# Kernel optimization log

Measured on AMD Instinct MI355X. Metric: run time of the kernel, lower is better.

The kernel has to match this reference:

```python
import jax, jax.numpy as jnp
import numpy as np

IN_DIM, HID, NCLS = 384, 16, 2
BN_EPS = 1e-5

def setup_inputs() -> dict:
    key = jax.random.key(0)
    ks = jax.random.split(key, 10)
    N, E, G = 50000, 200000, 64
    x = jax.random.normal(ks[0], (N, IN_DIM), dtype=jnp.float32)
    edge_index = jax.random.randint(ks[1], (2, E), 0, N, dtype=jnp.int64)
    batch = jnp.sort(jax.random.randint(ks[2], (N,), 0, G, dtype=jnp.int64))
    s1 = 1.0 / np.sqrt(2 * IN_DIM)
    s2 = 1.0 / np.sqrt(IN_DIM)
    s3 = 1.0 / np.sqrt(HID)
    lin_l_w = jax.random.uniform(ks[3], (HID, 2 * IN_DIM), minval=-s1, maxval=s1, dtype=jnp.float32)
    lin_l_b = jax.random.uniform(ks[4], (HID,), minval=-s1, maxval=s1, dtype=jnp.float32)
    lin_r_w = jax.random.uniform(ks[5], (HID, IN_DIM), minval=-s2, maxval=s2, dtype=jnp.float32)
    bn_gamma = jnp.ones((HID,), dtype=jnp.float32)
    bn_beta = jnp.zeros((HID,), dtype=jnp.float32)
    fc_w = jax.random.uniform(ks[6], (NCLS, HID), minval=-s3, maxval=s3, dtype=jnp.float32)
    fc_b = jax.random.uniform(ks[7], (NCLS,), minval=-s3, maxval=s3, dtype=jnp.float32)
    return {"x": x, "edge_index": edge_index, "batch": batch, "num_graphs": G,
            "lin_l_w": lin_l_w, "lin_l_b": lin_l_b, "lin_r_w": lin_r_w,
            "bn_gamma": bn_gamma, "bn_beta": bn_beta, "fc_w": fc_w, "fc_b": fc_b}

def reference(x, edge_index, batch, num_graphs, lin_l_w, lin_l_b, lin_r_w, bn_gamma, bn_beta, fc_w, fc_b):
    N = x.shape[0]
    # flow='target_to_source': aggregate x[edge_index[1]] (j) onto edge_index[0] (i)
    i, j = edge_index[0], edge_index[1]
    msg = x[j]                                                    # [E, IN_DIM]
    sum_agg = jax.ops.segment_sum(msg, i, num_segments=N)        # [N, IN_DIM]
    cnt = jax.ops.segment_sum(jnp.ones((msg.shape[0],), x.dtype), i, num_segments=N)
    mean_agg = sum_agg / jnp.clip(cnt, 1.0)[:, None]
    max_agg = jax.ops.segment_max(msg, i, num_segments=N)        # -inf where empty
    max_agg = jnp.where(jnp.isfinite(max_agg), max_agg, 0.0)     # PyG leaves 0 for isolated nodes
    agg = jnp.concatenate([mean_agg, max_agg], axis=-1)          # [N, 2*IN_DIM] (MultiAggregation cat)
    h = agg @ lin_l_w.T + lin_l_b + x @ lin_r_w.T                # SAGEConv: lin_l(aggr) + lin_r(root)
    # BatchNorm1d, training-mode batch statistics (biased variance)
    mu = jnp.mean(h, axis=0)
    var = jnp.mean(jnp.square(h - mu), axis=0)
    h = (h - mu) * jax.lax.rsqrt(var + BN_EPS) * bn_gamma + bn_beta
    h = jax.nn.relu(h)                                           # [N, HID]; hierarchical cat of 1 layer = h
    # global_mean_pool
    pooled_sum = jax.ops.segment_sum(h, batch, num_segments=num_graphs)
    gcnt = jax.ops.segment_sum(jnp.ones((N,), h.dtype), batch, num_segments=num_graphs)
    pooled = pooled_sum / jnp.clip(gcnt, 1.0)[:, None]           # [G, HID]
    return pooled @ fc_w.T + fc_b                                # [G, NCLS]
```

## Files before the change

kernel.cpp:

```cpp
#include <hip/hip_runtime.h>
#include <hip/hip_bf16.h>
#include <math.h>

#define IN_DIM 384
#define HID 16
#define NCLS 2
#define BN_EPS 1e-5f
#define MAXG 64
#define SLOTS 64

typedef __attribute__((ext_vector_type(8))) short bf16x8;
typedef __attribute__((ext_vector_type(4))) float f32x4;

__device__ __forceinline__ unsigned packbf(float a, float b) {
    __hip_bfloat162 h2 = __float22bfloat162_rn(make_float2(a, b));
    union { __hip_bfloat162 h; unsigned u; } c;
    c.h = h2;
    return c.u;
}

__global__ __launch_bounds__(256) void k_scatproj(const int* __restrict__ ei,
                                                  const int* __restrict__ ej, int E,
                                                  int* __restrict__ cnt,
                                                  int* __restrict__ colidx, int sblocks,
                                                  const float* __restrict__ x,
                                                  const float* __restrict__ wl,
                                                  const float* __restrict__ wr,
                                                  int N, float* __restrict__ y) {
    if ((int)blockIdx.x < sblocks) {
        int e = blockIdx.x * 256 + threadIdx.x;
        if (e < E) {
            int i = ei[e];
            int pos = atomicAdd(&cnt[i], 1);
            if (pos < SLOTS) colidx[(size_t)i * SLOTS + pos] = ej[e];
        }
        return;
    }
    int lane = threadIdx.x & 63;
    int ntiles = (N + 15) >> 4;
    int npairs = (ntiles + 1) >> 1;
    int pair = (blockIdx.x - sblocks) * 4 + (threadIdx.x >> 6);
    if (pair >= npairs) return;
    int t0 = pair * 2;
    int t1 = min(t0 + 1, ntiles - 1);
    bool two = (t0 + 1 < ntiles);
    int row = lane & 15;
    int g = lane >> 4;
    int node0 = t0 * 16 + row, node1 = t1 * 16 + row;
    int nc0 = min(node0, N - 1), nc1 = min(node1, N - 1);
    bool ok0 = (node0 < N), ok1 = two && (node1 < N);
    const float* xr0 = x + (size_t)nc0 * IN_DIM + g * 8;
    const float* xr1 = x + (size_t)nc1 * IN_DIM + g * 8;
    const float* wmr = wl + (size_t)row * (2 * IN_DIM) + g * 8;
    const float* wrr = wr + (size_t)row * IN_DIM + g * 8;
    f32x4 a0m = {0.f, 0.f, 0.f, 0.f}, a0r = a0m, a1m = a0m, a1r = a0m;
#pragma unroll
    for (int c = 0; c < 12; c++) {
        float4 ma = *(const float4*)(wmr + c * 32);
        float4 mc = *(const float4*)(wmr + c * 32 + 4);
        float4 ra = *(const float4*)(wrr + c * 32);
        float4 rc = *(const float4*)(wrr + c * 32 + 4);
        float4 p0 = *(const float4*)(xr0 + c * 32);
        float4 q0 = *(const float4*)(xr0 + c * 32 + 4);
        float4 p1 = *(const float4*)(xr1 + c * 32);
        float4 q1 = *(const float4*)(xr1 + c * 32 + 4);
        union { uint4 u; bf16x8 v; } wa, wb, x0, x1;
        wa.u.x = packbf(ma.x, ma.y); wa.u.y = packbf(ma.z, ma.w);
        wa.u.z = packbf(mc.x, mc.y); wa.u.w = packbf(mc.z, mc.w);
        wb.u.x = packbf(ra.x, ra.y); wb.u.y = packbf(ra.z, ra.w);
        wb.u.z = packbf(rc.x, rc.y); wb.u.w = packbf(rc.z, rc.w);
        x0.u.x = packbf(p0.x, p0.y); x0.u.y = packbf(p0.z, p0.w);
        x0.u.z = packbf(q0.x, q0.y); x0.u.w = packbf(q0.z, q0.w);
        x1.u.x = packbf(p1.x, p1.y); x1.u.y = packbf(p1.z, p1.w);
        x1.u.z = packbf(q1.x, q1.y); x1.u.w = packbf(q1.z, q1.w);
        a0m = __builtin_amdgcn_mfma_f32_16x16x32_bf16(wa.v, x0.v, a0m, 0, 0, 0);
        a0r = __builtin_amdgcn_mfma_f32_16x16x32_bf16(wb.v, x0.v, a0r, 0, 0, 0);
        a1m = __builtin_amdgcn_mfma_f32_16x16x32_bf16(wa.v, x1.v, a1m, 0, 0, 0);
        a1r = __builtin_amdgcn_mfma_f32_16x16x32_bf16(wb.v, x1.v, a1r, 0, 0, 0);
    }
    if (ok0) {
        float* yo = y + (size_t)node0 * 32 + g * 4;
        *(float4*)yo = make_float4(a0m[0], a0m[1], a0m[2], a0m[3]);
        *(float4*)(yo + 16) = make_float4(a0r[0], a0r[1], a0r[2], a0r[3]);
    }
    if (ok1) {
        float* yo = y + (size_t)node1 * 32 + g * 4;
        *(float4*)yo = make_float4(a1m[0], a1m[1], a1m[2], a1m[3]);
        *(float4*)(yo + 16) = make_float4(a1r[0], a1r[1], a1r[2], a1r[3]);
    }
}

__global__ __launch_bounds__(256) void k_node(const float* __restrict__ x,
                                              const float* __restrict__ y,
                                              const float* __restrict__ wl,
                                              const float* __restrict__ lb,
                                              const int* __restrict__ cnt,
                                              const int* __restrict__ colidx, int N,
                                              float* __restrict__ h,
                                              float* __restrict__ stats) {
    __shared__ float shS[32];
    if (threadIdx.x < 32) shS[threadIdx.x] = 0.f;
    __syncthreads();
    int lane = threadIdx.x & 63;
    int wid = threadIdx.x >> 6;
    int kq = ((lane >> 4) << 2) + (lane & 3);
    int nq = (lane & 15) >> 2;
    int slot = lane >> 4;
    int ch = lane & 15;
    const float* xl = x + 2 * lane;
    float sAcc = 0.f, s2Acc = 0.f;
    int ngroups = (N + 3) >> 2;
    int g = blockIdx.x * 4 + wid;
    if (g < ngroups) {
        int ibase = g << 2;
        int jpre[4];
        int dgv[4];
#pragma unroll
        for (int n = 0; n < 4; n++) {
            int i = ibase + n;
            dgv[n] = (i < N) ? min(cnt[i], SLOTS) : 0;
        }
#pragma unroll
        for (int n = 0; n < 4; n++) {
            int i = ibase + n;
            jpre[n] = (dgv[n] > 0) ? colidx[(size_t)i * SLOTS + min(lane, dgv[n] - 1)] : 0;
        }
        float2 mx[4][3];
        float sd[4];
#pragma unroll
        for (int n = 0; n < 4; n++) {
            int dg = dgv[n];
            float2 m0 = make_float2(-INFINITY, -INFINITY), m1 = m0, m2 = m0;
            float s = 0.f;
            int jv = jpre[n];
            for (int eb = 0; eb < dg; eb += 4) {
                int j0 = __shfl(jv, eb, 64);
                int j1 = __shfl(jv, eb + 1, 64);
                int j2 = __shfl(jv, eb + 2, 64);
                int j3 = __shfl(jv, eb + 3, 64);
                const float* p0 = xl + (size_t)j0 * IN_DIM;
                const float* p1 = xl + (size_t)j1 * IN_DIM;
                const float* p2 = xl + (size_t)j2 * IN_DIM;
                const float* p3 = xl + (size_t)j3 * IN_DIM;
                float2 a00 = *(const float2*)p0, a01 = *(const float2*)(p0 + 128),
                       a02 = *(const float2*)(p0 + 256);
                float2 a10 = *(const float2*)p1, a11 = *(const float2*)(p1 + 128),
                       a12 = *(const float2*)(p1 + 256);
                float2 a20 = *(const float2*)p2, a21 = *(const float2*)(p2 + 128),
                       a22 = *(const float2*)(p2 + 256);
                float2 a30 = *(const float2*)p3, a31 = *(const float2*)(p3 + 128),
                       a32 = *(const float2*)(p3 + 256);
                int js = (slot == 0) ? j0 : (slot == 1) ? j1 : (slot == 2) ? j2 : j3;
                float yv = y[(size_t)js * 32 + ch];
                s += (eb + slot < dg) ? yv : 0.f;
                m0.x = fmaxf(fmaxf(m0.x, fmaxf(a00.x, a10.x)), fmaxf(a20.x, a30.x));
                m0.y = fmaxf(fmaxf(m0.y, fmaxf(a00.y, a10.y)), fmaxf(a20.y, a30.y));
                m1.x = fmaxf(fmaxf(m1.x, fmaxf(a01.x, a11.x)), fmaxf(a21.x, a31.x));
                m1.y = fmaxf(fmaxf(m1.y, fmaxf(a01.y, a11.y)), fmaxf(a21.y, a31.y));
                m2.x = fmaxf(fmaxf(m2.x, fmaxf(a02.x, a12.x)), fmaxf(a22.x, a32.x));
                m2.y = fmaxf(fmaxf(m2.y, fmaxf(a02.y, a12.y)), fmaxf(a22.y, a32.y));
            }
            if (dg == 0) {
                m0 = make_float2(0.f, 0.f); m1 = m0; m2 = m0;
            }
            mx[n][0] = m0; mx[n][1] = m1; mx[n][2] = m2;
            sd[n] = s;
        }
#pragma unroll
        for (int n = 0; n < 4; n++) {
            sd[n] += __shfl_xor(sd[n], 16, 64);
            sd[n] += __shfl_xor(sd[n], 32, 64);
        }
        const float* wp = wl + IN_DIM + 2 * lane;
        float outv = 0.f;
#pragma unroll
        for (int kg = 0; kg < 4; kg++) {
            float r[16];
#pragma unroll
            for (int kk = 0; kk < 4; kk++) {
                int k = (kg << 2) + kk;
                const float* wrow = wp + (size_t)k * (2 * IN_DIM);
                float2 w0 = *(const float2*)wrow;
                float2 w1 = *(const float2*)(wrow + 128);
                float2 w2 = *(const float2*)(wrow + 256);
#pragma unroll
                for (int n = 0; n < 4; n++) {
                    float t = mx[n][0].x * w0.x;
                    t = fmaf(mx[n][0].y, w0.y, t);
                    t = fmaf(mx[n][1].x, w1.x, t);
                    t = fmaf(mx[n][1].y, w1.y, t);
                    t = fmaf(mx[n][2].x, w2.x, t);
                    t = fmaf(mx[n][2].y, w2.y, t);
                    r[(n << 2) + kk] = t;
                }
            }
#pragma unroll
            for (int st = 0; st < 4; st++) {
                int step = 1 << st;
                bool hi = (lane & step) != 0;
#pragma unroll
                for (int m = 0; m < (8 >> st); m++) {
                    float a = r[2 * m], b = r[2 * m + 1];
                    float send = hi ? a : b;
                    float keep = hi ? b : a;
                    r[m] = keep + __shfl_xor(send, step, 64);
                }
            }
            float v = r[0];
            v += __shfl_xor(v, 16, 64);
            v += __shfl_xor(v, 32, 64);
            if ((lane >> 4) == kg) outv = v;
        }
        int iw = ibase + nq;
        float t0 = __shfl(sd[0], kq, 64), t1 = __shfl(sd[1], kq, 64);
        float t2 = __shfl(sd[2], kq, 64), t3 = __shfl(sd[3], kq, 64);
        float sv = (nq == 0) ? t0 : (nq == 1) ? t1 : (nq == 2) ? t2 : t3;
        int dgs = (nq == 0) ? dgv[0] : (nq == 1) ? dgv[1] : (nq == 2) ? dgv[2] : dgv[3];
        if (iw < N) {
            float mean = sv / (float)max(dgs, 1);
            float hv = mean + outv + y[(size_t)iw * 32 + 16 + kq] + lb[kq];
            h[(size_t)iw * HID + kq] = hv;
            sAcc += hv;
            s2Acc = fmaf(hv, hv, s2Acc);
        }
    }
    __syncthreads();
    atomicAdd(&shS[kq], sAcc);
    atomicAdd(&shS[16 + kq], s2Acc);
    __syncthreads();
    if (threadIdx.x < 32) atomicAdd(&stats[threadIdx.x], shS[threadIdx.x]);
}

__global__ __launch_bounds__(256) void k_pool(const float* __restrict__ h,
                                              const int* __restrict__ batch,
                                              const float* __restrict__ stats,
                                              const float* __restrict__ gamma,
                                              const float* __restrict__ beta, int N,
                                              float* __restrict__ pooled,
                                              int* __restrict__ gcnt,
                                              int* __restrict__ ticket,
                                              const float* __restrict__ fcw,
                                              const float* __restrict__ fcb, int G,
                                              float* __restrict__ out) {
    __shared__ float smP[MAXG * HID];
    __shared__ int smC[MAXG];
    __shared__ int isLast;
    for (int idx = threadIdx.x; idx < MAXG * HID; idx += blockDim.x) smP[idx] = 0.f;
    if (threadIdx.x < MAXG) smC[threadIdx.x] = 0;
    __syncthreads();
    int c = threadIdx.x & 15;
    float invN = 1.f / (float)N;
    float mu = stats[c] * invN;
    float var = stats[16 + c] * invN - mu * mu;
    float sc = gamma[c] * rsqrtf(var + BN_EPS);
    float sh = beta[c] - mu * sc;
    int base = blockIdx.x * 256;
    int endn = min(base + 256, N);
    for (int idx = base * HID + threadIdx.x; idx < endn * HID; idx += blockDim.x) {
        int n = idx >> 4;
        float v = fmaxf(fmaf(h[idx], sc, sh), 0.f);
        int g = batch[n] & (MAXG - 1);
        atomicAdd(&smP[g * HID + c], v);
        if (c == 0) atomicAdd(&smC[g], 1);
    }
    __syncthreads();
    for (int idx = threadIdx.x; idx < MAXG * HID; idx += blockDim.x)
        if (smP[idx] != 0.f) atomicAdd(&pooled[idx], smP[idx]);
    if (threadIdx.x < MAXG && smC[threadIdx.x]) atomicAdd(&gcnt[threadIdx.x], smC[threadIdx.x]);
    __threadfence();
    __syncthreads();
    if (threadIdx.x == 0) {
        int t = atomicAdd(ticket, 1);
        isLast = (t == (int)gridDim.x - 1);
    }
    __syncthreads();
    if (isLast && threadIdx.x < G) {
        int g = threadIdx.x;
        __threadfence();
        int cntg = atomicAdd(&gcnt[g], 0);
        float inv = 1.f / (float)max(cntg, 1);
        float o0 = fcb[0], o1 = fcb[1];
#pragma unroll
        for (int chh = 0; chh < HID; chh++) {
            float pv = atomicAdd(&pooled[g * HID + chh], 0.f) * inv;
            o0 = fmaf(pv, fcw[chh], o0);
            o1 = fmaf(pv, fcw[HID + chh], o1);
        }
        out[g * NCLS + 0] = o0;
        out[g * NCLS + 1] = o1;
    }
}

extern "C" void kernel_launch(void* const* d_in, const int* in_sizes, int n_in,
                              void* d_out, int out_size, void* d_ws, size_t ws_size,
                              hipStream_t stream) {
    const float* x = (const float*)d_in[0];
    const int* ei = (const int*)d_in[1];
    const int* batch = (const int*)d_in[2];
    const float* wl = (const float*)d_in[4];
    const float* lb = (const float*)d_in[5];
    const float* wr = (const float*)d_in[6];
    const float* gamma = (const float*)d_in[7];
    const float* beta = (const float*)d_in[8];
    const float* fcw = (const float*)d_in[9];
    const float* fcb = (const float*)d_in[10];

    const int N = in_sizes[0] / IN_DIM;
    const int E = in_sizes[1] / 2;
    const int G = out_size / NCLS;
    const int* ej = ei + E;

    size_t off = 0;
    auto take = [&](size_t b) { size_t r = off; off += (b + 255) & ~(size_t)255; return r; };
    size_t cnt_off  = take((size_t)N * 4);
    size_t stat_off = take(32 * 4);
    size_t pool_off = take((size_t)MAXG * HID * 4);
    size_t gcnt_off = take((size_t)MAXG * 4);
    size_t tick_off = take(4);
    size_t zero_bytes = off;
    size_t col_off  = take((size_t)N * SLOTS * 4);
    size_t y_off    = take((size_t)N * 32 * 4);
    size_t h_off    = take((size_t)N * HID * 4);
    (void)ws_size;

    char* ws = (char*)d_ws;
    int* cnt = (int*)(ws + cnt_off);
    float* stats = (float*)(ws + stat_off);
    float* pooled = (float*)(ws + pool_off);
    int* gcnt = (int*)(ws + gcnt_off);
    int* ticket = (int*)(ws + tick_off);
    int* colidx = (int*)(ws + col_off);
    float* y = (float*)(ws + y_off);
    float* h = (float*)(ws + h_off);

    hipMemsetAsync(d_ws, 0, zero_bytes, stream);

    int eblocks = (E + 255) / 256;
    int ngroups = (N + 3) >> 2;
    int gblocks = (ngroups + 3) / 4;
    int ntiles = (N + 15) >> 4;
    int npairs = (ntiles + 1) >> 1;
    int pblocks = (npairs + 3) / 4;
    k_scatproj<<<eblocks + pblocks, 256, 0, stream>>>(ei, ej, E, cnt, colidx, eblocks,
                                                      x, wl, wr, N, y);
    k_node<<<gblocks, 256, 0, stream>>>(x, y, wl, lb, cnt, colidx, N, h, stats);
    k_pool<<<(N + 255) / 256, 256, 0, stream>>>(h, batch, stats, gamma, beta, N, pooled,
                                                gcnt, ticket, fcw, fcb, G, (float*)d_out);
}
```

Before: 130.7 us.

## Rebalance scatter/projection block split and shrink node-kernel blocks

The fused scatter+projection kernel now places projection blocks first and uses a fixed set of 256 grid-stride scatter blocks instead of one block per 256 edges. Each projection wave now handles one 16-node tile instead of two, which doubles the number of waves and halves per-wave register use. The node kernel drops from 256 to 128 threads per block, giving more, smaller blocks. Together these aim to balance work across CUs and reduce scheduling imbalance between the atomic scatter and the MFMA projection, at the cost of less weight reuse per wave.

```diff
diff --git a/kernel.cpp b/kernel.cpp
--- a/kernel.cpp
+++ b/kernel.cpp
@@ -8,6 +8,7 @@
 #define BN_EPS 1e-5f
 #define MAXG 64
 #define SLOTS 64
+#define SCATB 256
 
 typedef __attribute__((ext_vector_type(8))) short bf16x8;
 typedef __attribute__((ext_vector_type(4))) float f32x4;
@@ -22,14 +23,14 @@
 __global__ __launch_bounds__(256) void k_scatproj(const int* __restrict__ ei,
                                                   const int* __restrict__ ej, int E,
                                                   int* __restrict__ cnt,
-                                                  int* __restrict__ colidx, int sblocks,
+                                                  int* __restrict__ colidx, int pblocks,
                                                   const float* __restrict__ x,
                                                   const float* __restrict__ wl,
                                                   const float* __restrict__ wr,
                                                   int N, float* __restrict__ y) {
-    if ((int)blockIdx.x < sblocks) {
-        int e = blockIdx.x * 256 + threadIdx.x;
-        if (e < E) {
+    if ((int)blockIdx.x >= pblocks) {
+        int stride = SCATB * 256;
+        for (int e = (blockIdx.x - pblocks) * 256 + threadIdx.x; e < E; e += stride) {
             int i = ei[e];
             int pos = atomicAdd(&cnt[i], 1);
             if (pos < SLOTS) colidx[(size_t)i * SLOTS + pos] = ej[e];
@@ -37,60 +38,45 @@
         return;
     }
     int lane = threadIdx.x & 63;
+    int tile = blockIdx.x * 4 + (threadIdx.x >> 6);
     int ntiles = (N + 15) >> 4;
-    int npairs = (ntiles + 1) >> 1;
-    int pair = (blockIdx.x - sblocks) * 4 + (threadIdx.x >> 6);
-    if (pair >= npairs) return;
-    int t0 = pair * 2;
-    int t1 = min(t0 + 1, ntiles - 1);
-    bool two = (t0 + 1 < ntiles);
+    if (tile >= ntiles) return;
     int row = lane & 15;
     int g = lane >> 4;
-    int node0 = t0 * 16 + row, node1 = t1 * 16 + row;
-    int nc0 = min(node0, N - 1), nc1 = min(node1, N - 1);
-    bool ok0 = (node0 < N), ok1 = two && (node1 < N);
-    const float* xr0 = x + (size_t)nc0 * IN_DIM + g * 8;
-    const float* xr1 = x + (size_t)nc1 * IN_DIM + g * 8;
+    int node = tile * 16 + row;
+    int nodec = min(node, N - 1);
+    bool ok = (node < N);
+    const float* xr = x + (size_t)nodec * IN_DIM + g * 8;
     const float* wmr = wl + (size_t)row * (2 * IN_DIM) + g * 8;
     const float* wrr = wr + (size_t)row * IN_DIM + g * 8;
-    f32x4 a0m = {0.f, 0.f, 0.f, 0.f}, a0r = a0m, a1m = a0m, a1r = a0m;
+    f32x4 acc0 = {0.f, 0.f, 0.f, 0.f};
+    f32x4 acc1 = {0.f, 0.f, 0.f, 0.f};
 #pragma unroll
     for (int c = 0; c < 12; c++) {
+        float4 xa = *(const float4*)(xr + c * 32);
+        float4 xc = *(const float4*)(xr + c * 32 + 4);
         float4 ma = *(const float4*)(wmr + c * 32);
         float4 mc = *(const float4*)(wmr + c * 32 + 4);
         float4 ra = *(const float4*)(wrr + c * 32);
         float4 rc = *(const float4*)(wrr + c * 32 + 4);
-        float4 p0 = *(const float4*)(xr0 + c * 32);
-        float4 q0 = *(const float4*)(xr0 + c * 32 + 4);
-        float4 p1 = *(const float4*)(xr1 + c * 32);
-        float4 q1 = *(const float4*)(xr1 + c * 32 + 4);
-        union { uint4 u; bf16x8 v; } wa, wb, x0, x1;
+        union { uint4 u; bf16x8 v; } xf, wa, wb;
+        xf.u.x = packbf(xa.x, xa.y); xf.u.y = packbf(xa.z, xa.w);
+        xf.u.z = packbf(xc.x, xc.y); xf.u.w = packbf(xc.z, xc.w);
         wa.u.x = packbf(ma.x, ma.y); wa.u.y = packbf(ma.z, ma.w);
         wa.u.z = packbf(mc.x, mc.y); wa.u.w = packbf(mc.z, mc.w);
         wb.u.x = packbf(ra.x, ra.y); wb.u.y = packbf(ra.z, ra.w);
         wb.u.z = packbf(rc.x, rc.y); wb.u.w = packbf(rc.z, rc.w);
-        x0.u.x = packbf(p0.x, p0.y); x0.u.y = packbf(p0.z, p0.w);
-        x0.u.z = packbf(q0.x, q0.y); x0.u.w = packbf(q0.z, q0.w);
-        x1.u.x = packbf(p1.x, p1.y); x1.u.y = packbf(p1.z, p1.w);
-        x1.u.z = packbf(q1.x, q1.y); x1.u.w = packbf(q1.z, q1.w);
-        a0m = __builtin_amdgcn_mfma_f32_16x16x32_bf16(wa.v, x0.v, a0m, 0, 0, 0);
-        a0r = __builtin_amdgcn_mfma_f32_16x16x32_bf16(wb.v, x0.v, a0r, 0, 0, 0);
-        a1m = __builtin_amdgcn_mfma_f32_16x16x32_bf16(wa.v, x1.v, a1m, 0, 0, 0);
-        a1r = __builtin_amdgcn_mfma_f32_16x16x32_bf16(wb.v, x1.v, a1r, 0, 0, 0);
-    }
-    if (ok0) {
-        float* yo = y + (size_t)node0 * 32 + g * 4;
-        *(float4*)yo = make_float4(a0m[0], a0m[1], a0m[2], a0m[3]);
-        *(float4*)(yo + 16) = make_float4(a0r[0], a0r[1], a0r[2], a0r[3]);
-    }
-    if (ok1) {
-        float* yo = y + (size_t)node1 * 32 + g * 4;
-        *(float4*)yo = make_float4(a1m[0], a1m[1], a1m[2], a1m[3]);
-        *(float4*)(yo + 16) = make_float4(a1r[0], a1r[1], a1r[2], a1r[3]);
-    }
-}
-
-__global__ __launch_bounds__(256) void k_node(const float* __restrict__ x,
+        acc0 = __builtin_amdgcn_mfma_f32_16x16x32_bf16(wa.v, xf.v, acc0, 0, 0, 0);
+        acc1 = __builtin_amdgcn_mfma_f32_16x16x32_bf16(wb.v, xf.v, acc1, 0, 0, 0);
+    }
+    if (ok) {
+        float* yo = y + (size_t)node * 32 + g * 4;
+        *(float4*)yo = make_float4(acc0[0], acc0[1], acc0[2], acc0[3]);
+        *(float4*)(yo + 16) = make_float4(acc1[0], acc1[1], acc1[2], acc1[3]);
+    }
+}
+
+__global__ __launch_bounds__(128) void k_node(const float* __restrict__ x,
                                               const float* __restrict__ y,
                                               const float* __restrict__ wl,
                                               const float* __restrict__ lb,
@@ -110,7 +96,7 @@
     const float* xl = x + 2 * lane;
     float sAcc = 0.f, s2Acc = 0.f;
     int ngroups = (N + 3) >> 2;
-    int g = blockIdx.x * 4 + wid;
+    int g = blockIdx.x * 2 + wid;
     if (g < ngroups) {
         int ibase = g << 2;
         int jpre[4];
@@ -335,15 +321,12 @@
 
     hipMemsetAsync(d_ws, 0, zero_bytes, stream);
 
-    int eblocks = (E + 255) / 256;
     int ngroups = (N + 3) >> 2;
-    int gblocks = (ngroups + 3) / 4;
     int ntiles = (N + 15) >> 4;
-    int npairs = (ntiles + 1) >> 1;
-    int pblocks = (npairs + 3) / 4;
-    k_scatproj<<<eblocks + pblocks, 256, 0, stream>>>(ei, ej, E, cnt, colidx, eblocks,
-                                                      x, wl, wr, N, y);
-    k_node<<<gblocks, 256, 0, stream>>>(x, y, wl, lb, cnt, colidx, N, h, stats);
+    int pblocks = (ntiles + 3) / 4;
+    k_scatproj<<<pblocks + SCATB, 256, 0, stream>>>(ei, ej, E, cnt, colidx, pblocks,
+                                                    x, wl, wr, N, y);
+    k_node<<<(ngroups + 1) / 2, 128, 0, stream>>>(x, y, wl, lb, cnt, colidx, N, h, stats);
     k_pool<<<(N + 255) / 256, 256, 0, stream>>>(h, batch, stats, gamma, beta, N, pooled,
                                                 gcnt, ticket, fcw, fcb, G, (float*)d_out);
 }
```

Measured after the change: 171.1 us. 31.0% more time.
